# Kernel optimization log

Hardware: AMD Instinct MI355X
Metric: run time of the kernel (lower is better)

The kernel has to match this reference:

```python
import jax, jax.numpy as jnp
import numpy as np

L = 2048  # sequence length (number of atoms)
B = 8     # batch size


def setup_inputs() -> dict:
    key = jax.random.key(0)
    kx, ky, km = jax.random.split(key, 3)
    x = jax.random.normal(kx, (L, B, 3), dtype=jnp.float32) * 5.0
    y = jax.random.normal(ky, (L, B, 3), dtype=jnp.float32) * 5.0
    # mask values ARE indices (source: idx = mask[i][mask[i] != 0]).
    # Per-sample permutation of [0, L): exactly one zero entry per sample is
    # dropped by the mask!=0 filter, so every sample selects n = L-1 distinct rows.
    perms = jax.vmap(lambda k: jax.random.permutation(k, L))(jax.random.split(km, B))  # (B, L)
    mask = perms.T.astype(jnp.int32)  # (L, B)
    return {"x": x, "y": y, "mask": mask}


def _pair_dist(p):
    # p: (n, 3) -> (n, n) pairwise Euclidean distances
    sq = jnp.sum(p * p, axis=-1)                      # (n,)
    d = sq[:, None] + sq[None, :] - 2.0 * (p @ p.T)   # squared distances
    d = d - jnp.diag(jnp.diag(d))                     # exact-zero diagonal (as in source)
    d = jnp.maximum(d, 0.0)                           # relu
    pos = d > 0
    # safe sqrt: identical forward values, avoids nan grads at exact zeros
    return jnp.sqrt(jnp.where(pos, d, 1.0)) * pos


def reference(x, y, mask):
    xb = jnp.transpose(x, (1, 0, 2))  # (B, L, 3)
    yb = jnp.transpose(y, (1, 0, 2))
    mb = mask.T                        # (B, L)
    # drop the single zero per sample; order is irrelevant for dRMSD
    idx = jnp.sort(mb, axis=1)[:, 1:]  # (B, n) with n = L-1, distinct indices
    xs = jnp.take_along_axis(xb, idx[..., None], axis=1)  # (B, n, 3)
    ys = jnp.take_along_axis(yb, idx[..., None], axis=1)
    xd = jax.vmap(_pair_dist)(xs)      # (B, n, n)
    yd = jax.vmap(_pair_dist)(ys)
    D = yd - xd
    n = idx.shape[1]
    norms = jnp.sqrt(jnp.sum(D * D, axis=(1, 2)))          # per-sample Frobenius norm
    drmsd = jnp.sum(norms) / jnp.sqrt(jnp.float32(n * n - n)) / xb.shape[0]
    return drmsd.reshape(1)
```

## Files before the change

kernel.cpp:

```cpp
#include <hip/hip_runtime.h>
#include <math.h>

#define L 2048
#define B 8
#define N 2047
#define BLOCK 256
#define II 2
#define ITILE (BLOCK * II)
#define JC 64
#define UNITS 80
#define NBLOCKS (UNITS * B)

__device__ double g_part[NBLOCKS];
__device__ unsigned int g_ticket = 0;

__device__ __forceinline__ float fsqrt_fast(float v) {
    float r;
    asm("v_sqrt_f32 %0, %1" : "=v"(r) : "v"(v));
    return r;
}

__launch_bounds__(BLOCK)
__global__ void drmsd_kernel(const float* __restrict__ x, const float* __restrict__ y,
                             float* __restrict__ out) {
    __shared__ float4 ldsx[JC], ldsy[JC];
    __shared__ float wsum[BLOCK / 64];
    __shared__ int amlast;
    __shared__ double fsum8[B];

    const int bx  = blockIdx.x;
    const int b   = blockIdx.y;
    const int tid = threadIdx.x;

    int ti, jc;
    if (bx < 32)      { ti = 0; jc = bx;      }
    else if (bx < 56) { ti = 1; jc = bx - 24; }
    else if (bx < 72) { ti = 2; jc = bx - 40; }
    else              { ti = 3; jc = bx - 48; }

    if (tid < JC) {
        int row = jc * JC + tid + 1;
        if (row > L - 1) row = L - 1;
        int base = (row * B + b) * 3;
        ldsx[tid] = make_float4(x[base], x[base + 1], x[base + 2], 0.f);
        ldsy[tid] = make_float4(y[base], y[base + 1], y[base + 2], 0.f);
    }

    float xi[II][3], yi[II][3], accf[II];
    bool valid[II];
#pragma unroll
    for (int k = 0; k < II; ++k) {
        int i = ti * ITILE + k * BLOCK + tid;
        valid[k] = (i < N);
        int row = i + 1; if (row > L - 1) row = L - 1;
        int base = (row * B + b) * 3;
        xi[k][0] = x[base]; xi[k][1] = x[base + 1]; xi[k][2] = x[base + 2];
        yi[k][0] = y[base]; yi[k][1] = y[base + 1]; yi[k][2] = y[base + 2];
        accf[k] = 0.f;
    }
    __syncthreads();

    const int jmax = min(JC, N - jc * JC);
#pragma unroll 4
    for (int jj = 0; jj < jmax; ++jj) {
        float4 xj = ldsx[jj];
        float4 yj = ldsy[jj];
#pragma unroll
        for (int k = 0; k < II; ++k) {
            float dx0 = xi[k][0] - xj.x, dx1 = xi[k][1] - xj.y, dx2 = xi[k][2] - xj.z;
            float dy0 = yi[k][0] - yj.x, dy1 = yi[k][1] - yj.y, dy2 = yi[k][2] - yj.z;
            float dxs = dx0 * dx0 + dx1 * dx1 + dx2 * dx2;
            float dys = dy0 * dy0 + dy1 * dy1 + dy2 * dy2;
            float t = fsqrt_fast(dys) - fsqrt_fast(dxs);
            accf[k] += t * t;
        }
    }

    float tot = 0.f;
#pragma unroll
    for (int k = 0; k < II; ++k) tot += valid[k] ? accf[k] : 0.f;

#pragma unroll
    for (int off = 32; off > 0; off >>= 1)
        tot += __shfl_down(tot, off, 64);

    int lane = tid & 63, wv = tid >> 6;
    if (lane == 0) wsum[wv] = tot;
    __syncthreads();

    if (tid == 0) {
        double s = (double)wsum[0] + (double)wsum[1] + (double)wsum[2] + (double)wsum[3];
        double w = (jc < 8 * (ti + 1)) ? 1.0 : 2.0;
        g_part[b * UNITS + bx] = w * s;
        __threadfence();
        unsigned int old = atomicAdd(&g_ticket, 1u);
        amlast = ((old % NBLOCKS) == NBLOCKS - 1) ? 1 : 0;
    }
    __syncthreads();

    if (amlast) {
        __threadfence();
        int s8 = tid >> 5, g = tid & 31;
        const double* p = g_part + s8 * UNITS;
        double v = __hip_atomic_load(p + g,      __ATOMIC_RELAXED, __HIP_MEMORY_SCOPE_AGENT)
                 + __hip_atomic_load(p + g + 32, __ATOMIC_RELAXED, __HIP_MEMORY_SCOPE_AGENT);
        if (g < UNITS - 64)
            v += __hip_atomic_load(p + g + 64, __ATOMIC_RELAXED, __HIP_MEMORY_SCOPE_AGENT);
#pragma unroll
        for (int off = 16; off > 0; off >>= 1)
            v += __shfl_down(v, off, 32);
        if (g == 0) fsum8[s8] = sqrt(v);
        __syncthreads();
        if (tid == 0) {
            double t = 0.0;
#pragma unroll
            for (int q = 0; q < B; ++q) t += fsum8[q];
            double denom = sqrt((double)N * (double)N - (double)N) * (double)B;
            out[0] = (float)(t / denom);
        }
    }
}

extern "C" void kernel_launch(void* const* d_in, const int* in_sizes, int n_in,
                              void* d_out, int out_size, void* d_ws, size_t ws_size,
                              hipStream_t stream) {
    const float* x = (const float*)d_in[0];
    const float* y = (const float*)d_in[1];
    float* out = (float*)d_out;

    dim3 grid(UNITS, B);
    drmsd_kernel<<<grid, BLOCK, 0, stream>>>(x, y, out);
}
```

Before: 79.73 us.

## Use single-sqrt pair identity and triangular masking on diagonal tiles

Replaces (sqrt(dy)-sqrt(dx))^2 with dx+dy-2*sqrt(dx*dy), accumulating the sum and root terms separately so each pair needs one square root instead of two. Diagonal tiles now evaluate only the strict upper triangle per wave via predicated loop variants, and the factor of two is applied once at the final reduction instead of per block. This reduces transcendental work and skips redundant pair evaluations, at the cost of possible float cancellation when the two distances are close and more code variants.

```diff
diff --git a/kernel.cpp b/kernel.cpp
--- a/kernel.cpp
+++ b/kernel.cpp
@@ -46,7 +46,7 @@
         ldsy[tid] = make_float4(y[base], y[base + 1], y[base + 2], 0.f);
     }
 
-    float xi[II][3], yi[II][3], accf[II];
+    float xi[II][3], yi[II][3], accA[II], accB[II];
     bool valid[II];
 #pragma unroll
     for (int k = 0; k < II; ++k) {
@@ -56,42 +56,64 @@
         int base = (row * B + b) * 3;
         xi[k][0] = x[base]; xi[k][1] = x[base + 1]; xi[k][2] = x[base + 2];
         yi[k][0] = y[base]; yi[k][1] = y[base + 1]; yi[k][2] = y[base + 2];
-        accf[k] = 0.f;
+        accA[k] = 0.f; accB[k] = 0.f;
     }
     __syncthreads();
 
     const int jmax = min(JC, N - jc * JC);
-#pragma unroll 4
-    for (int jj = 0; jj < jmax; ++jj) {
-        float4 xj = ldsx[jj];
-        float4 yj = ldsy[jj];
-#pragma unroll
-        for (int k = 0; k < II; ++k) {
-            float dx0 = xi[k][0] - xj.x, dx1 = xi[k][1] - xj.y, dx2 = xi[k][2] - xj.z;
-            float dy0 = yi[k][0] - yj.x, dy1 = yi[k][1] - yj.y, dy2 = yi[k][2] - yj.z;
-            float dxs = dx0 * dx0 + dx1 * dx1 + dx2 * dx2;
-            float dys = dy0 * dy0 + dy1 * dy1 + dy2 * dy2;
-            float t = fsqrt_fast(dys) - fsqrt_fast(dxs);
-            accf[k] += t * t;
-        }
+    const int lane = tid & 63;
+    const int wv   = tid >> 6;
+
+    const int c = jc - 8 * ti;
+    int m0, m1;
+    if (c >= 8)      { m0 = 2; m1 = 2; }
+    else {
+        const int r0 = wv, r1 = 4 + wv;
+        m0 = (r0 < c) ? 2 : ((r0 == c) ? 1 : 0);
+        m1 = (r1 < c) ? 2 : ((r1 == c) ? 1 : 0);
     }
+
+#define PAIR_BODY(k, PRED) do {                                              \
+    float dx0 = xi[k][0] - xj.x, dx1 = xi[k][1] - xj.y, dx2 = xi[k][2] - xj.z; \
+    float dy0 = yi[k][0] - yj.x, dy1 = yi[k][1] - yj.y, dy2 = yi[k][2] - yj.z; \
+    float dxs = dx0 * dx0 + dx1 * dx1 + dx2 * dx2;                           \
+    float dys = dy0 * dy0 + dy1 * dy1 + dy2 * dy2;                           \
+    float s  = fsqrt_fast(dxs * dys);                                        \
+    float su = dxs + dys;                                                    \
+    if (PRED) { bool ok = jj > lane; su = ok ? su : 0.f; s = ok ? s : 0.f; } \
+    accA[k] += su; accB[k] += s;                                             \
+} while (0)
+
+#define PAIR_LOOP(M0, M1) do {                                               \
+    _Pragma("unroll 4")                                                      \
+    for (int jj = 0; jj < jmax; ++jj) {                                      \
+        float4 xj = ldsx[jj];                                                \
+        float4 yj = ldsy[jj];                                                \
+        if (M0) PAIR_BODY(0, (M0) == 1);                                     \
+        if (M1) PAIR_BODY(1, (M1) == 1);                                     \
+    }                                                                        \
+} while (0)
+
+    if (m1 == 2)      PAIR_LOOP(2, 2);
+    else if (m1 == 1) PAIR_LOOP(2, 1);
+    else if (m0 == 2) PAIR_LOOP(2, 0);
+    else if (m0 == 1) PAIR_LOOP(1, 0);
 
     float tot = 0.f;
 #pragma unroll
-    for (int k = 0; k < II; ++k) tot += valid[k] ? accf[k] : 0.f;
+    for (int k = 0; k < II; ++k)
+        tot += valid[k] ? fmaf(-2.f, accB[k], accA[k]) : 0.f;
 
 #pragma unroll
     for (int off = 32; off > 0; off >>= 1)
         tot += __shfl_down(tot, off, 64);
 
-    int lane = tid & 63, wv = tid >> 6;
     if (lane == 0) wsum[wv] = tot;
     __syncthreads();
 
     if (tid == 0) {
         double s = (double)wsum[0] + (double)wsum[1] + (double)wsum[2] + (double)wsum[3];
-        double w = (jc < 8 * (ti + 1)) ? 1.0 : 2.0;
-        g_part[b * UNITS + bx] = w * s;
+        g_part[b * UNITS + bx] = s;
         __threadfence();
         unsigned int old = atomicAdd(&g_ticket, 1u);
         amlast = ((old % NBLOCKS) == NBLOCKS - 1) ? 1 : 0;
@@ -109,7 +131,7 @@
 #pragma unroll
         for (int off = 16; off > 0; off >>= 1)
             v += __shfl_down(v, off, 32);
-        if (g == 0) fsum8[s8] = sqrt(v);
+        if (g == 0) fsum8[s8] = sqrt(2.0 * v);
         __syncthreads();
         if (tid == 0) {
             double t = 0.0;
```

Result: no change. 78.90 us (-1.0%).
